# Performance work log

Measured on AMD Instinct MI355X. Metric: run time of the kernel, lower is better.

## Reference

```python
import jax, jax.numpy as jnp
import numpy as np

B, N, F = 32, 1024, 7
HID, HID_GLO, MLP_H, OUT = 256, 8, 64, 8
THRESHOLD = 0.3


def setup_inputs() -> dict:
    key = jax.random.key(0)
    ks = jax.random.split(key, 16)
    def lin(k, fan_out, fan_in):
        # xavier-uniform-like init
        lim = (6.0 / (fan_in + fan_out)) ** 0.5
        return jax.random.uniform(k, (fan_out, fan_in), jnp.float32, -lim, lim)
    return {
        "x": jax.random.normal(ks[0], (B, N, F), jnp.float32),
        "W1": lin(ks[1], HID, 2),   "b1": jnp.zeros((HID,), jnp.float32),
        "W2": lin(ks[2], HID, HID), "b2": jnp.zeros((HID,), jnp.float32),
        "Wfc": lin(ks[3], HID, HID), "bfc": jnp.zeros((HID,), jnp.float32),
        "Wg": lin(ks[4], HID_GLO, 2), "bg": jnp.zeros((HID_GLO,), jnp.float32),
        "Wm0": lin(ks[5], MLP_H, N * F), "bm0": jnp.zeros((MLP_H,), jnp.float32),
        "Wm1": lin(ks[6], MLP_H, MLP_H), "bm1": jnp.zeros((MLP_H,), jnp.float32),
        "Wp": lin(ks[7], OUT, MLP_H + HID + HID_GLO), "bp": jnp.zeros((OUT,), jnp.float32),
    }


def reference(x, W1, b1, W2, b2, Wfc, bfc, Wg, bg, Wm0, bm0, Wm1, bm1, Wp, bp):
    # --- GCN branch (torch code detaches node features & adjacency) ---
    pts = jax.lax.stop_gradient(x[:, :, 1:3])                     # [B,N,2]
    diff = pts[:, :, None, :] - pts[:, None, :, :]                # [B,N,N,2]
    dist = jnp.sqrt(jnp.sum(diff * diff, axis=-1))                # [B,N,N]
    adj = (dist < THRESHOLD).astype(x.dtype)                      # [B,N,N]
    dinv = 1.0 / jnp.sqrt(jnp.sum(adj, axis=-1))                  # [B,N] (>=1, self-loop)
    nadj = dinv[:, :, None] * adj * dinv[:, None, :]              # D^-1/2 A D^-1/2
    h = jax.nn.relu(jnp.einsum('bij,bjd->bid', nadj, pts) @ W1.T + b1)   # [B,N,256]
    g = jnp.einsum('bij,bjh->bih', nadj, h) @ W2.T + b2                  # [B,N,256]
    gcn_en = jnp.mean(g, axis=1) @ Wfc.T + bfc                    # [B,256]

    # --- global branch (torch code uses .item() -> constants) ---
    v = jax.lax.stop_gradient(x[:, :, 1:5])                       # [B,N,4]
    avg_speed = jnp.mean(jnp.linalg.norm(v[:, :, 2:4], axis=-1), axis=1)  # [B]
    density = 1.0 / jnp.max(dist, axis=(1, 2))                    # [B] (v3 == pts)
    glo_in = jnp.stack([avg_speed, density], axis=-1)             # [B,2]
    glo_en = jax.nn.relu(glo_in @ Wg.T + bg)                      # [B,8]

    # --- MLP branch on flattened x ---
    xf = x.reshape(x.shape[0], -1)                                # [B, N*F]
    xf = jax.nn.relu(xf @ Wm0.T + bm0)
    xf = jax.nn.relu(xf @ Wm1.T + bm1)                            # [B,64]

    out = jnp.concatenate([xf, gcn_en, glo_en], axis=1) @ Wp.T + bp  # [B,8]
    return out
```

## Files before the change

### kernel.cpp

```cpp
#include <hip/hip_runtime.h>

#define BB 32
#define NN 1024
#define FF 7
#define HID 256
#define MLPH 64
#define OUTN 8
#define CATN (MLPH + HID + 8)

__device__ __forceinline__ float wave_sum(float v) {
#pragma unroll
    for (int m = 32; m >= 1; m >>= 1) v += __shfl_xor(v, m, 64);
    return v;
}
__device__ __forceinline__ float wave_max(float v) {
#pragma unroll
    for (int m = 32; m >= 1; m >>= 1) v = fmaxf(v, __shfl_xor(v, m, 64));
    return v;
}

union S1 {
    struct { float xb[NN * FF]; float l0[NN], l1[NN], s2[NN], s3[NN]; float wred[16]; } a;
    struct { float xb[NN * FF]; float wred[16]; } p;
    struct { float l0[HID], l1[HID], r2[HID]; float wred[16]; } c;
    struct { float wb[NN * FF]; } m;
};

__global__ __launch_bounds__(1024, 4) void k1(const float* __restrict__ x,
                                              const float* __restrict__ Wm0,
                                              const float* __restrict__ W2,
                                              const float* __restrict__ b2,
                                              const float* __restrict__ Wfc,
                                              const float* __restrict__ bfc,
                                              const float* __restrict__ Wp,
                                              float* __restrict__ pts0,
                                              float* __restrict__ pts1,
                                              float* __restrict__ spd,
                                              float* __restrict__ mlp_p,
                                              float* __restrict__ E,
                                              float* __restrict__ cE,
                                              float* __restrict__ deg,
                                              float* __restrict__ bmaxp,
                                              float* __restrict__ out) {
    __shared__ __align__(16) S1 sm;
    int blk = blockIdx.x, tid = threadIdx.x, lane = tid & 63, w = tid >> 6;
    if (blk < 256) {
        int b = blk >> 3, jg = blk & 7;
        const float4* xr = (const float4*)(x + b * (NN * FF));
        float4* s4 = (float4*)sm.a.xb;
        for (int i = tid; i < 1792; i += 1024) s4[i] = xr[i];
        __syncthreads();
        sm.a.l0[tid] = sm.a.xb[tid * FF + 1];
        sm.a.l1[tid] = sm.a.xb[tid * FF + 2];
        __syncthreads();
        int jA = jg * 128 + lane, jB = jA + 64;
        float pj0a = sm.a.l0[jA], pj1a = sm.a.l1[jA];
        float pj0b = sm.a.l0[jB], pj1b = sm.a.l1[jB];
        const float4* v0p = (const float4*)&sm.a.l0[w * 64];
        const float4* v1p = (const float4*)&sm.a.l1[w * 64];
        unsigned dA = 0u, dB = 0u;
        float mx = 0.f;
#pragma unroll 4
        for (int g = 0; g < 16; ++g) {
            float4 v0 = v0p[g], v1 = v1p[g];
            float dx, dy, d2a, d2b;
            dx = pj0a - v0.x; dy = pj1a - v1.x; d2a = fmaf(dy, dy, dx * dx);
            dx = pj0b - v0.x; dy = pj1b - v1.x; d2b = fmaf(dy, dy, dx * dx);
            dA += (d2a <= 0.09f); dB += (d2b <= 0.09f);
            mx = fmaxf(mx, fmaxf(d2a, d2b));
            dx = pj0a - v0.y; dy = pj1a - v1.y; d2a = fmaf(dy, dy, dx * dx);
            dx = pj0b - v0.y; dy = pj1b - v1.y; d2b = fmaf(dy, dy, dx * dx);
            dA += (d2a <= 0.09f); dB += (d2b <= 0.09f);
            mx = fmaxf(mx, fmaxf(d2a, d2b));
            dx = pj0a - v0.z; dy = pj1a - v1.z; d2a = fmaf(dy, dy, dx * dx);
            dx = pj0b - v0.z; dy = pj1b - v1.z; d2b = fmaf(dy, dy, dx * dx);
            dA += (d2a <= 0.09f); dB += (d2b <= 0.09f);
            mx = fmaxf(mx, fmaxf(d2a, d2b));
            dx = pj0a - v0.w; dy = pj1a - v1.w; d2a = fmaf(dy, dy, dx * dx);
            dx = pj0b - v0.w; dy = pj1b - v1.w; d2b = fmaf(dy, dy, dx * dx);
            dA += (d2a <= 0.09f); dB += (d2b <= 0.09f);
            mx = fmaxf(mx, fmaxf(d2a, d2b));
        }
        sm.a.s2[tid] = (float)dA;
        sm.a.s3[tid] = (float)dB;
        mx = wave_max(mx);
        if (lane == 0) sm.a.wred[w] = mx;
        __syncthreads();
        if (tid < 64) {
            float s = 0.f;
#pragma unroll
            for (int kk = 0; kk < 16; ++kk) s += sm.a.s2[kk * 64 + tid];
            deg[b * NN + jg * 128 + tid] = s;
        } else if (tid < 128) {
            int t = tid - 64;
            float s = 0.f;
#pragma unroll
            for (int kk = 0; kk < 16; ++kk) s += sm.a.s3[kk * 64 + t];
            deg[b * NN + jg * 128 + 64 + t] = s;
        }
        if (tid == 0) {
            float m = sm.a.wred[0];
#pragma unroll
            for (int i = 1; i < 16; ++i) m = fmaxf(m, sm.a.wred[i]);
            bmaxp[b * 8 + jg] = m;
        }
    } else if (blk < 288) {
        int b = blk - 256;
        const float4* xr = (const float4*)(x + b * (NN * FF));
        float4* s4 = (float4*)sm.p.xb;
        for (int i = tid; i < 1792; i += 1024) s4[i] = xr[i];
        if (tid < OUTN) out[b * OUTN + tid] = 0.f;
        __syncthreads();
        pts0[b * NN + tid] = sm.p.xb[tid * FF + 1];
        pts1[b * NN + tid] = sm.p.xb[tid * FF + 2];
        float vx = sm.p.xb[tid * FF + 3], vy = sm.p.xb[tid * FF + 4];
        float sp = sqrtf(fmaf(vx, vx, vy * vy));
        sp = wave_sum(sp);
        if (lane == 0) sm.p.wred[w] = sp;
        __syncthreads();
        if (tid == 0) {
            float s = 0.f;
#pragma unroll
            for (int i = 0; i < 16; ++i) s += sm.p.wred[i];
            spd[b] = s;
        }
    } else if (blk < 296) {
        int o = blk - 288;
        if (tid < HID) sm.c.l0[tid] = Wp[o * CATN + MLPH + tid];
        __syncthreads();
        if (tid < HID) {
            float a = 0.f;
#pragma unroll 8
            for (int m = 0; m < HID; ++m) a = fmaf(sm.c.l0[m], Wfc[m * HID + tid], a);
            sm.c.l1[tid] = a;
            sm.c.r2[tid] = sm.c.l0[tid] * bfc[tid];
        }
        __syncthreads();
        if (tid < HID) {
            float e = 0.f;
#pragma unroll 8
            for (int k = 0; k < HID; ++k) e = fmaf(sm.c.l1[k], W2[k * HID + tid], e);
            E[o * HID + tid] = e;
            float c = fmaf(sm.c.l1[tid], b2[tid], sm.c.r2[tid]);
            c = wave_sum(c);
            if (lane == 0) sm.c.wred[w] = c;
        }
        __syncthreads();
        if (tid == 0) cE[o] = sm.c.wred[0] + sm.c.wred[1] + sm.c.wred[2] + sm.c.wred[3];
    } else {
        int t = blk - 296, h = t >> 1, half = t & 1;
        const float4* wr = (const float4*)(Wm0 + h * (NN * FF));
        float4* s4 = (float4*)sm.m.wb;
        for (int i = tid; i < 1792; i += 1024) s4[i] = wr[i];
        __syncthreads();
        int b = half * 16 + w;
        const float4* xr = (const float4*)(x + b * (NN * FF));
        float4 a4 = {0.f, 0.f, 0.f, 0.f};
#pragma unroll 7
        for (int it = 0; it < 28; ++it) {
            float4 xv = xr[it * 64 + lane];
            float4 wv = s4[it * 64 + lane];
            a4.x = fmaf(wv.x, xv.x, a4.x);
            a4.y = fmaf(wv.y, xv.y, a4.y);
            a4.z = fmaf(wv.z, xv.z, a4.z);
            a4.w = fmaf(wv.w, xv.w, a4.w);
        }
        float s = (a4.x + a4.y) + (a4.z + a4.w);
        s = wave_sum(s);
        if (lane == 0) mlp_p[b * MLPH + h] = s;
    }
}

struct S2 {
    float l0[NN], l1[NN], di[NN];
    float r0a[NN], r1a[NN], r2a[NN], r0b[NN], r1b[NN], r2b[NN];
    float q0[128], q1[128], qw[128];
};

__global__ __launch_bounds__(1024, 4) void k2(const float* __restrict__ pts0,
                                              const float* __restrict__ pts1,
                                              const float* __restrict__ deg,
                                              const float* __restrict__ W1,
                                              const float* __restrict__ b1,
                                              const float* __restrict__ Wg,
                                              const float* __restrict__ bg,
                                              const float* __restrict__ Wm1,
                                              const float* __restrict__ bm1,
                                              const float* __restrict__ Wp,
                                              const float* __restrict__ bp,
                                              const float* __restrict__ bm0,
                                              const float* __restrict__ mlp_p,
                                              const float* __restrict__ bmaxp,
                                              const float* __restrict__ spd,
                                              const float* __restrict__ E,
                                              const float* __restrict__ cE,
                                              float* __restrict__ out) {
    __shared__ __align__(16) S2 sm;
    int blk = blockIdx.x, tid = threadIdx.x, lane = tid & 63, w = tid >> 6;
    int b = blk >> 3, jg = blk & 7;
    float* hsl  = sm.l0;
    float* sx1  = sm.l1;
    float* sxf2 = sm.l1 + 64;
    float* sglo = sm.l1 + 128;
    sm.l0[tid] = pts0[b * NN + tid];
    sm.l1[tid] = pts1[b * NN + tid];
    sm.di[tid] = 1.0f / sqrtf(deg[b * NN + tid]);
    __syncthreads();
    int jA = jg * 128 + lane, jB = jA + 64;
    float pj0a = sm.l0[jA], pj1a = sm.l1[jA];
    float pj0b = sm.l0[jB], pj1b = sm.l1[jB];
    const float4* v0p = (const float4*)&sm.l0[w * 64];
    const float4* v1p = (const float4*)&sm.l1[w * 64];
    const float4* vdp = (const float4*)&sm.di[w * 64];
    float a0a = 0.f, a1a = 0.f, asa = 0.f;
    float a0b = 0.f, a1b = 0.f, asb = 0.f;
#pragma unroll 4
    for (int g = 0; g < 16; ++g) {
        float4 v0 = v0p[g], v1 = v1p[g], vd = vdp[g];
        float dx, dy, d2, t;
        dx = pj0a - v0.x; dy = pj1a - v1.x; d2 = fmaf(dy, dy, dx * dx);
        t = (d2 <= 0.09f) ? vd.x : 0.0f;
        a0a = fmaf(t, v0.x, a0a); a1a = fmaf(t, v1.x, a1a); asa += t;
        dx = pj0b - v0.x; dy = pj1b - v1.x; d2 = fmaf(dy, dy, dx * dx);
        t = (d2 <= 0.09f) ? vd.x : 0.0f;
        a0b = fmaf(t, v0.x, a0b); a1b = fmaf(t, v1.x, a1b); asb += t;
        dx = pj0a - v0.y; dy = pj1a - v1.y; d2 = fmaf(dy, dy, dx * dx);
        t = (d2 <= 0.09f) ? vd.y : 0.0f;
        a0a = fmaf(t, v0.y, a0a); a1a = fmaf(t, v1.y, a1a); asa += t;
        dx = pj0b - v0.y; dy = pj1b - v1.y; d2 = fmaf(dy, dy, dx * dx);
        t = (d2 <= 0.09f) ? vd.y : 0.0f;
        a0b = fmaf(t, v0.y, a0b); a1b = fmaf(t, v1.y, a1b); asb += t;
        dx = pj0a - v0.z; dy = pj1a - v1.z; d2 = fmaf(dy, dy, dx * dx);
        t = (d2 <= 0.09f) ? vd.z : 0.0f;
        a0a = fmaf(t, v0.z, a0a); a1a = fmaf(t, v1.z, a1a); asa += t;
        dx = pj0b - v0.z; dy = pj1b - v1.z; d2 = fmaf(dy, dy, dx * dx);
        t = (d2 <= 0.09f) ? vd.z : 0.0f;
        a0b = fmaf(t, v0.z, a0b); a1b = fmaf(t, v1.z, a1b); asb += t;
        dx = pj0a - v0.w; dy = pj1a - v1.w; d2 = fmaf(dy, dy, dx * dx);
        t = (d2 <= 0.09f) ? vd.w : 0.0f;
        a0a = fmaf(t, v0.w, a0a); a1a = fmaf(t, v1.w, a1a); asa += t;
        dx = pj0b - v0.w; dy = pj1b - v1.w; d2 = fmaf(dy, dy, dx * dx);
        t = (d2 <= 0.09f) ? vd.w : 0.0f;
        a0b = fmaf(t, v0.w, a0b); a1b = fmaf(t, v1.w, a1b); asb += t;
    }
    sm.r0a[tid] = a0a; sm.r1a[tid] = a1a; sm.r2a[tid] = asa;
    sm.r0b[tid] = a0b; sm.r1b[tid] = a1b; sm.r2b[tid] = asb;
    __syncthreads();
    if (tid < 128) {
        int t = tid & 63;
        const float* R0 = (tid < 64) ? sm.r0a : sm.r0b;
        const float* R1 = (tid < 64) ? sm.r1a : sm.r1b;
        const float* R2 = (tid < 64) ? sm.r2a : sm.r2b;
        int j = jg * 128 + tid;
        float s0 = 0.f, s1 = 0.f, ss = 0.f;
#pragma unroll
        for (int kk = 0; kk < 16; ++kk) {
            s0 += R0[kk * 64 + t];
            s1 += R1[kk * 64 + t];
            ss += R2[kk * 64 + t];
        }
        float dj = sm.di[j];
        sm.q0[tid] = dj * s0;
        sm.q1[tid] = dj * s1;
        sm.qw[tid] = dj * ss * (1.0f / NN);
    } else if (jg == 0 && tid < 192) {
        int t2 = tid - 128;
        sx1[t2] = fmaxf(mlp_p[b * MLPH + t2] + bm0[t2], 0.f);
    }
    __syncthreads();
    {
        int h = tid & 255, jq = tid >> 8;
        float w10 = W1[2 * h], w11 = W1[2 * h + 1], bb = b1[h];
        const float4* q0v = (const float4*)&sm.q0[jq * 32];
        const float4* q1v = (const float4*)&sm.q1[jq * 32];
        const float4* qwv = (const float4*)&sm.qw[jq * 32];
        float acc = 0.f;
#pragma unroll
        for (int g = 0; g < 8; ++g) {
            float4 qa = q0v[g], qb = q1v[g], qw4 = qwv[g];
            acc = fmaf(qw4.x, fmaxf(fmaf(qb.x, w11, fmaf(qa.x, w10, bb)), 0.f), acc);
            acc = fmaf(qw4.y, fmaxf(fmaf(qb.y, w11, fmaf(qa.y, w10, bb)), 0.f), acc);
            acc = fmaf(qw4.z, fmaxf(fmaf(qb.z, w11, fmaf(qa.z, w10, bb)), 0.f), acc);
            acc = fmaf(qw4.w, fmaxf(fmaf(qb.w, w11, fmaf(qa.w, w10, bb)), 0.f), acc);
        }
        sm.r0a[jq * 256 + h] = acc;
    }
    __syncthreads();
    if (tid < HID) {
        hsl[tid] = sm.r0a[tid] + sm.r0a[256 + tid] + sm.r0a[512 + tid] + sm.r0a[768 + tid];
    } else if (jg == 0 && tid < HID + MLPH) {
        int t2 = tid - HID;
        float a = bm1[t2];
        const float* wv = Wm1 + t2 * MLPH;
#pragma unroll
        for (int k = 0; k < MLPH; ++k) a = fmaf(wv[k], sx1[k], a);
        sxf2[t2] = fmaxf(a, 0.f);
    } else if (jg == 0 && tid < HID + MLPH + 8) {
        int t2 = tid - HID - MLPH;
        float mx = 0.f;
#pragma unroll
        for (int g = 0; g < 8; ++g) mx = fmaxf(mx, bmaxp[b * 8 + g]);
        float avg  = spd[b] * (1.0f / NN);
        float dens = 1.0f / sqrtf(mx);
        sglo[t2] = fmaxf(fmaf(Wg[t2 * 2], avg, fmaf(Wg[t2 * 2 + 1], dens, bg[t2])), 0.f);
    }
    __syncthreads();
    if (tid < 512) {
        int o = tid >> 6, ln = tid & 63;
        const float* Eo = E + o * HID;
        float a = Eo[ln] * hsl[ln];
        a = fmaf(Eo[ln + 64],  hsl[ln + 64],  a);
        a = fmaf(Eo[ln + 128], hsl[ln + 128], a);
        a = fmaf(Eo[ln + 192], hsl[ln + 192], a);
        if (jg == 0) a = fmaf(Wp[o * CATN + ln], sxf2[ln], a);
        a = wave_sum(a);
        if (ln == 0) {
            if (jg == 0) {
                const float* wg = Wp + o * CATN + MLPH + HID;
#pragma unroll
                for (int g = 0; g < 8; ++g) a = fmaf(wg[g], sglo[g], a);
                a += cE[o] + bp[o];
            }
            atomicAdd(&out[b * OUTN + o], a);
        }
    }
}

extern "C" void kernel_launch(void* const* d_in, const int* in_sizes, int n_in,
                              void* d_out, int out_size, void* d_ws, size_t ws_size,
                              hipStream_t stream) {
    const float* x   = (const float*)d_in[0];
    const float* W1  = (const float*)d_in[1];
    const float* b1  = (const float*)d_in[2];
    const float* W2  = (const float*)d_in[3];
    const float* b2  = (const float*)d_in[4];
    const float* Wfc = (const float*)d_in[5];
    const float* bfc = (const float*)d_in[6];
    const float* Wg  = (const float*)d_in[7];
    const float* bg  = (const float*)d_in[8];
    const float* Wm0 = (const float*)d_in[9];
    const float* bm0 = (const float*)d_in[10];
    const float* Wm1 = (const float*)d_in[11];
    const float* bm1 = (const float*)d_in[12];
    const float* Wp  = (const float*)d_in[13];
    const float* bp  = (const float*)d_in[14];
    float* out = (float*)d_out;
    float* ws  = (float*)d_ws;

    float* pts0  = ws;
    float* pts1  = ws + 32768;
    float* deg   = ws + 65536;
    float* mlp_p = ws + 98304;
    float* bmaxp = ws + 100352;
    float* spd   = ws + 100608;
    float* E     = ws + 100640;
    float* cE    = ws + 102688;

    k1<<<424, 1024, 0, stream>>>(x, Wm0, W2, b2, Wfc, bfc, Wp,
                                 pts0, pts1, spd, mlp_p, E, cE, deg, bmaxp, out);
    k2<<<256, 1024, 0, stream>>>(pts0, pts1, deg, W1, b1, Wg, bg, Wm1, bm1,
                                 Wp, bp, bm0, mlp_p, bmaxp, spd, E, cE, out);
}
```

Before: 123.5 us.

## Merge heterogeneous k1 block roles into uniform 512-thread blocks and drop pts buffers

Replaces the 424-block heterogeneous first kernel with 256 uniform 512-thread blocks. Each block now computes its degree slice, one MLP layer-0 dot product per wave, and optionally the speed sum and E precompute. The second kernel reads point coordinates straight from x instead of from pts0/pts1 workspace buffers, and both kernels halve their thread count and double the per-thread loop length. This is meant to cut the block count, the extra global round trip and the shared-memory footprint, at the cost of uncoalesced strided reads of x and Wm0 being reread per batch without shared staging.

```diff
diff --git a/kernel.cpp b/kernel.cpp
--- a/kernel.cpp
+++ b/kernel.cpp
@@ -1,6 +1,5 @@
 #include <hip/hip_runtime.h>
 
-#define BB 32
 #define NN 1024
 #define FF 7
 #define HID 256
@@ -19,203 +18,190 @@
     return v;
 }
 
-union S1 {
-    struct { float xb[NN * FF]; float l0[NN], l1[NN], s2[NN], s3[NN]; float wred[16]; } a;
-    struct { float xb[NN * FF]; float wred[16]; } p;
-    struct { float l0[HID], l1[HID], r2[HID]; float wred[16]; } c;
-    struct { float wb[NN * FF]; } m;
-};
-
-__global__ __launch_bounds__(1024, 4) void k1(const float* __restrict__ x,
-                                              const float* __restrict__ Wm0,
-                                              const float* __restrict__ W2,
-                                              const float* __restrict__ b2,
-                                              const float* __restrict__ Wfc,
-                                              const float* __restrict__ bfc,
-                                              const float* __restrict__ Wp,
-                                              float* __restrict__ pts0,
-                                              float* __restrict__ pts1,
-                                              float* __restrict__ spd,
-                                              float* __restrict__ mlp_p,
-                                              float* __restrict__ E,
-                                              float* __restrict__ cE,
-                                              float* __restrict__ deg,
-                                              float* __restrict__ bmaxp,
-                                              float* __restrict__ out) {
-    __shared__ __align__(16) S1 sm;
+__global__ __launch_bounds__(512, 4) void g1(const float* __restrict__ x,
+                                             const float* __restrict__ Wm0,
+                                             const float* __restrict__ W2,
+                                             const float* __restrict__ b2,
+                                             const float* __restrict__ Wfc,
+                                             const float* __restrict__ bfc,
+                                             const float* __restrict__ Wp,
+                                             float* __restrict__ spd,
+                                             float* __restrict__ mlp_p,
+                                             float* __restrict__ E,
+                                             float* __restrict__ cE,
+                                             float* __restrict__ deg,
+                                             float* __restrict__ bmaxp,
+                                             float* __restrict__ out) {
+    __shared__ __align__(16) float l0[NN];
+    __shared__ __align__(16) float l1[NN];
+    __shared__ __align__(16) float s2[8 * 128];
+    __shared__ float wred[8];
+    __shared__ float eg0[HID];
+    __shared__ float eg1[HID];
     int blk = blockIdx.x, tid = threadIdx.x, lane = tid & 63, w = tid >> 6;
-    if (blk < 256) {
-        int b = blk >> 3, jg = blk & 7;
-        const float4* xr = (const float4*)(x + b * (NN * FF));
-        float4* s4 = (float4*)sm.a.xb;
-        for (int i = tid; i < 1792; i += 1024) s4[i] = xr[i];
-        __syncthreads();
-        sm.a.l0[tid] = sm.a.xb[tid * FF + 1];
-        sm.a.l1[tid] = sm.a.xb[tid * FF + 2];
-        __syncthreads();
-        int jA = jg * 128 + lane, jB = jA + 64;
-        float pj0a = sm.a.l0[jA], pj1a = sm.a.l1[jA];
-        float pj0b = sm.a.l0[jB], pj1b = sm.a.l1[jB];
-        const float4* v0p = (const float4*)&sm.a.l0[w * 64];
-        const float4* v1p = (const float4*)&sm.a.l1[w * 64];
-        unsigned dA = 0u, dB = 0u;
-        float mx = 0.f;
+    int b = blk >> 3, jg = blk & 7;
+    const float* xb = x + b * (NN * FF);
+    {
+        int j0 = tid, j1 = tid + 512;
+        l0[j0] = xb[j0 * FF + 1]; l1[j0] = xb[j0 * FF + 2];
+        l0[j1] = xb[j1 * FF + 1]; l1[j1] = xb[j1 * FF + 2];
+    }
+    __syncthreads();
+    int jA = jg * 128 + lane, jB = jA + 64;
+    float pj0a = l0[jA], pj1a = l1[jA];
+    float pj0b = l0[jB], pj1b = l1[jB];
+    const float4* v0p = (const float4*)&l0[w * 128];
+    const float4* v1p = (const float4*)&l1[w * 128];
+    unsigned dA = 0u, dB = 0u;
+    float mx = 0.f;
 #pragma unroll 4
-        for (int g = 0; g < 16; ++g) {
-            float4 v0 = v0p[g], v1 = v1p[g];
-            float dx, dy, d2a, d2b;
-            dx = pj0a - v0.x; dy = pj1a - v1.x; d2a = fmaf(dy, dy, dx * dx);
-            dx = pj0b - v0.x; dy = pj1b - v1.x; d2b = fmaf(dy, dy, dx * dx);
-            dA += (d2a <= 0.09f); dB += (d2b <= 0.09f);
-            mx = fmaxf(mx, fmaxf(d2a, d2b));
-            dx = pj0a - v0.y; dy = pj1a - v1.y; d2a = fmaf(dy, dy, dx * dx);
-            dx = pj0b - v0.y; dy = pj1b - v1.y; d2b = fmaf(dy, dy, dx * dx);
-            dA += (d2a <= 0.09f); dB += (d2b <= 0.09f);
-            mx = fmaxf(mx, fmaxf(d2a, d2b));
-            dx = pj0a - v0.z; dy = pj1a - v1.z; d2a = fmaf(dy, dy, dx * dx);
-            dx = pj0b - v0.z; dy = pj1b - v1.z; d2b = fmaf(dy, dy, dx * dx);
-            dA += (d2a <= 0.09f); dB += (d2b <= 0.09f);
-            mx = fmaxf(mx, fmaxf(d2a, d2b));
-            dx = pj0a - v0.w; dy = pj1a - v1.w; d2a = fmaf(dy, dy, dx * dx);
-            dx = pj0b - v0.w; dy = pj1b - v1.w; d2b = fmaf(dy, dy, dx * dx);
-            dA += (d2a <= 0.09f); dB += (d2b <= 0.09f);
-            mx = fmaxf(mx, fmaxf(d2a, d2b));
-        }
-        sm.a.s2[tid] = (float)dA;
-        sm.a.s3[tid] = (float)dB;
-        mx = wave_max(mx);
-        if (lane == 0) sm.a.wred[w] = mx;
-        __syncthreads();
-        if (tid < 64) {
-            float s = 0.f;
-#pragma unroll
-            for (int kk = 0; kk < 16; ++kk) s += sm.a.s2[kk * 64 + tid];
-            deg[b * NN + jg * 128 + tid] = s;
-        } else if (tid < 128) {
-            int t = tid - 64;
-            float s = 0.f;
-#pragma unroll
-            for (int kk = 0; kk < 16; ++kk) s += sm.a.s3[kk * 64 + t];
-            deg[b * NN + jg * 128 + 64 + t] = s;
-        }
-        if (tid == 0) {
-            float m = sm.a.wred[0];
-#pragma unroll
-            for (int i = 1; i < 16; ++i) m = fmaxf(m, sm.a.wred[i]);
-            bmaxp[b * 8 + jg] = m;
-        }
-    } else if (blk < 288) {
-        int b = blk - 256;
-        const float4* xr = (const float4*)(x + b * (NN * FF));
-        float4* s4 = (float4*)sm.p.xb;
-        for (int i = tid; i < 1792; i += 1024) s4[i] = xr[i];
+    for (int g = 0; g < 32; ++g) {
+        float4 v0 = v0p[g], v1 = v1p[g];
+        float dx, dy, d2a, d2b;
+        dx = pj0a - v0.x; dy = pj1a - v1.x; d2a = fmaf(dy, dy, dx * dx);
+        dx = pj0b - v0.x; dy = pj1b - v1.x; d2b = fmaf(dy, dy, dx * dx);
+        dA += (d2a <= 0.09f); dB += (d2b <= 0.09f);
+        mx = fmaxf(mx, fmaxf(d2a, d2b));
+        dx = pj0a - v0.y; dy = pj1a - v1.y; d2a = fmaf(dy, dy, dx * dx);
+        dx = pj0b - v0.y; dy = pj1b - v1.y; d2b = fmaf(dy, dy, dx * dx);
+        dA += (d2a <= 0.09f); dB += (d2b <= 0.09f);
+        mx = fmaxf(mx, fmaxf(d2a, d2b));
+        dx = pj0a - v0.z; dy = pj1a - v1.z; d2a = fmaf(dy, dy, dx * dx);
+        dx = pj0b - v0.z; dy = pj1b - v1.z; d2b = fmaf(dy, dy, dx * dx);
+        dA += (d2a <= 0.09f); dB += (d2b <= 0.09f);
+        mx = fmaxf(mx, fmaxf(d2a, d2b));
+        dx = pj0a - v0.w; dy = pj1a - v1.w; d2a = fmaf(dy, dy, dx * dx);
+        dx = pj0b - v0.w; dy = pj1b - v1.w; d2b = fmaf(dy, dy, dx * dx);
+        dA += (d2a <= 0.09f); dB += (d2b <= 0.09f);
+        mx = fmaxf(mx, fmaxf(d2a, d2b));
+    }
+    s2[w * 128 + lane] = (float)dA;
+    s2[w * 128 + 64 + lane] = (float)dB;
+    mx = wave_max(mx);
+    if (lane == 0) wred[w] = mx;
+    __syncthreads();
+    if (tid < 128) {
+        float s = 0.f;
+#pragma unroll
+        for (int kk = 0; kk < 8; ++kk) s += s2[kk * 128 + tid];
+        deg[b * NN + jg * 128 + tid] = s;
+    }
+    if (tid == 0) {
+        float m = wred[0];
+#pragma unroll
+        for (int i = 1; i < 8; ++i) m = fmaxf(m, wred[i]);
+        bmaxp[b * 8 + jg] = m;
+    }
+    {
+        int h = jg * 8 + w;
+        const float4* wr = (const float4*)(Wm0 + h * (NN * FF));
+        const float4* xr = (const float4*)xb;
+        float4 a4 = {0.f, 0.f, 0.f, 0.f};
+#pragma unroll 7
+        for (int it = 0; it < 28; ++it) {
+            float4 wv = wr[it * 64 + lane];
+            float4 xv = xr[it * 64 + lane];
+            a4.x = fmaf(wv.x, xv.x, a4.x);
+            a4.y = fmaf(wv.y, xv.y, a4.y);
+            a4.z = fmaf(wv.z, xv.z, a4.z);
+            a4.w = fmaf(wv.w, xv.w, a4.w);
+        }
+        float s = (a4.x + a4.y) + (a4.z + a4.w);
+        s = wave_sum(s);
+        if (lane == 0) mlp_p[b * MLPH + h] = s;
+    }
+    __syncthreads();
+    if (jg == 0) {
+        int j0 = tid, j1 = tid + 512;
+        float vx = xb[j0 * FF + 3], vy = xb[j0 * FF + 4];
+        float sp = sqrtf(fmaf(vx, vx, vy * vy));
+        vx = xb[j1 * FF + 3]; vy = xb[j1 * FF + 4];
+        sp += sqrtf(fmaf(vx, vx, vy * vy));
+        sp = wave_sum(sp);
+        if (lane == 0) wred[w] = sp;
         if (tid < OUTN) out[b * OUTN + tid] = 0.f;
-        __syncthreads();
-        pts0[b * NN + tid] = sm.p.xb[tid * FF + 1];
-        pts1[b * NN + tid] = sm.p.xb[tid * FF + 2];
-        float vx = sm.p.xb[tid * FF + 3], vy = sm.p.xb[tid * FF + 4];
-        float sp = sqrtf(fmaf(vx, vx, vy * vy));
-        sp = wave_sum(sp);
-        if (lane == 0) sm.p.wred[w] = sp;
-        __syncthreads();
-        if (tid == 0) {
-            float s = 0.f;
-#pragma unroll
-            for (int i = 0; i < 16; ++i) s += sm.p.wred[i];
-            spd[b] = s;
-        }
-    } else if (blk < 296) {
-        int o = blk - 288;
-        if (tid < HID) sm.c.l0[tid] = Wp[o * CATN + MLPH + tid];
+    }
+    __syncthreads();
+    if (jg == 0 && tid == 0) {
+        float s = 0.f;
+#pragma unroll
+        for (int i = 0; i < 8; ++i) s += wred[i];
+        spd[b] = s;
+    }
+    if (b < 8 && jg == 7) {
+        int o = b;
+        if (tid < HID) eg0[tid] = Wp[o * CATN + MLPH + tid];
         __syncthreads();
         if (tid < HID) {
             float a = 0.f;
 #pragma unroll 8
-            for (int m = 0; m < HID; ++m) a = fmaf(sm.c.l0[m], Wfc[m * HID + tid], a);
-            sm.c.l1[tid] = a;
-            sm.c.r2[tid] = sm.c.l0[tid] * bfc[tid];
+            for (int m = 0; m < HID; ++m) a = fmaf(eg0[m], Wfc[m * HID + tid], a);
+            eg1[tid] = a;
         }
         __syncthreads();
         if (tid < HID) {
             float e = 0.f;
 #pragma unroll 8
-            for (int k = 0; k < HID; ++k) e = fmaf(sm.c.l1[k], W2[k * HID + tid], e);
+            for (int k = 0; k < HID; ++k) e = fmaf(eg1[k], W2[k * HID + tid], e);
             E[o * HID + tid] = e;
-            float c = fmaf(sm.c.l1[tid], b2[tid], sm.c.r2[tid]);
+            float c = fmaf(eg1[tid], b2[tid], eg0[tid] * bfc[tid]);
             c = wave_sum(c);
-            if (lane == 0) sm.c.wred[w] = c;
+            if (lane == 0) wred[w] = c;
         }
         __syncthreads();
-        if (tid == 0) cE[o] = sm.c.wred[0] + sm.c.wred[1] + sm.c.wred[2] + sm.c.wred[3];
-    } else {
-        int t = blk - 296, h = t >> 1, half = t & 1;
-        const float4* wr = (const float4*)(Wm0 + h * (NN * FF));
-        float4* s4 = (float4*)sm.m.wb;
-        for (int i = tid; i < 1792; i += 1024) s4[i] = wr[i];
-        __syncthreads();
-        int b = half * 16 + w;
-        const float4* xr = (const float4*)(x + b * (NN * FF));
-        float4 a4 = {0.f, 0.f, 0.f, 0.f};
-#pragma unroll 7
-        for (int it = 0; it < 28; ++it) {
-            float4 xv = xr[it * 64 + lane];
-            float4 wv = s4[it * 64 + lane];
-            a4.x = fmaf(wv.x, xv.x, a4.x);
-            a4.y = fmaf(wv.y, xv.y, a4.y);
-            a4.z = fmaf(wv.z, xv.z, a4.z);
-            a4.w = fmaf(wv.w, xv.w, a4.w);
-        }
-        float s = (a4.x + a4.y) + (a4.z + a4.w);
-        s = wave_sum(s);
-        if (lane == 0) mlp_p[b * MLPH + h] = s;
-    }
-}
-
-struct S2 {
-    float l0[NN], l1[NN], di[NN];
-    float r0a[NN], r1a[NN], r2a[NN], r0b[NN], r1b[NN], r2b[NN];
-    float q0[128], q1[128], qw[128];
-};
-
-__global__ __launch_bounds__(1024, 4) void k2(const float* __restrict__ pts0,
-                                              const float* __restrict__ pts1,
-                                              const float* __restrict__ deg,
-                                              const float* __restrict__ W1,
-                                              const float* __restrict__ b1,
-                                              const float* __restrict__ Wg,
-                                              const float* __restrict__ bg,
-                                              const float* __restrict__ Wm1,
-                                              const float* __restrict__ bm1,
-                                              const float* __restrict__ Wp,
-                                              const float* __restrict__ bp,
-                                              const float* __restrict__ bm0,
-                                              const float* __restrict__ mlp_p,
-                                              const float* __restrict__ bmaxp,
-                                              const float* __restrict__ spd,
-                                              const float* __restrict__ E,
-                                              const float* __restrict__ cE,
-                                              float* __restrict__ out) {
-    __shared__ __align__(16) S2 sm;
+        if (tid == 0) cE[o] = wred[0] + wred[1] + wred[2] + wred[3];
+    }
+}
+
+__global__ __launch_bounds__(512, 4) void g2(const float* __restrict__ x,
+                                             const float* __restrict__ deg,
+                                             const float* __restrict__ W1,
+                                             const float* __restrict__ b1,
+                                             const float* __restrict__ Wg,
+                                             const float* __restrict__ bg,
+                                             const float* __restrict__ Wm1,
+                                             const float* __restrict__ bm1,
+                                             const float* __restrict__ Wp,
+                                             const float* __restrict__ bp,
+                                             const float* __restrict__ bm0,
+                                             const float* __restrict__ mlp_p,
+                                             const float* __restrict__ bmaxp,
+                                             const float* __restrict__ spd,
+                                             const float* __restrict__ E,
+                                             const float* __restrict__ cE,
+                                             float* __restrict__ out) {
+    __shared__ __align__(16) float l0[NN];
+    __shared__ __align__(16) float l1[NN];
+    __shared__ __align__(16) float di[NN];
+    __shared__ __align__(16) float r0[8 * 128];
+    __shared__ __align__(16) float r1[8 * 128];
+    __shared__ __align__(16) float r2[8 * 128];
+    __shared__ __align__(16) float q0s[128];
+    __shared__ __align__(16) float q1s[128];
+    __shared__ __align__(16) float qws[128];
+    __shared__ __align__(16) float hp[512];
+    __shared__ float sx1[MLPH], sxf2[MLPH], sglo[8];
     int blk = blockIdx.x, tid = threadIdx.x, lane = tid & 63, w = tid >> 6;
     int b = blk >> 3, jg = blk & 7;
-    float* hsl  = sm.l0;
-    float* sx1  = sm.l1;
-    float* sxf2 = sm.l1 + 64;
-    float* sglo = sm.l1 + 128;
-    sm.l0[tid] = pts0[b * NN + tid];
-    sm.l1[tid] = pts1[b * NN + tid];
-    sm.di[tid] = 1.0f / sqrtf(deg[b * NN + tid]);
+    const float* xb = x + b * (NN * FF);
+    {
+        int j0 = tid, j1 = tid + 512;
+        l0[j0] = xb[j0 * FF + 1]; l1[j0] = xb[j0 * FF + 2];
+        l0[j1] = xb[j1 * FF + 1]; l1[j1] = xb[j1 * FF + 2];
+        di[j0] = 1.0f / sqrtf(deg[b * NN + j0]);
+        di[j1] = 1.0f / sqrtf(deg[b * NN + j1]);
+    }
     __syncthreads();
     int jA = jg * 128 + lane, jB = jA + 64;
-    float pj0a = sm.l0[jA], pj1a = sm.l1[jA];
-    float pj0b = sm.l0[jB], pj1b = sm.l1[jB];
-    const float4* v0p = (const float4*)&sm.l0[w * 64];
-    const float4* v1p = (const float4*)&sm.l1[w * 64];
-    const float4* vdp = (const float4*)&sm.di[w * 64];
+    float pj0a = l0[jA], pj1a = l1[jA];
+    float pj0b = l0[jB], pj1b = l1[jB];
+    const float4* v0p = (const float4*)&l0[w * 128];
+    const float4* v1p = (const float4*)&l1[w * 128];
+    const float4* vdp = (const float4*)&di[w * 128];
     float a0a = 0.f, a1a = 0.f, asa = 0.f;
     float a0b = 0.f, a1b = 0.f, asb = 0.f;
 #pragma unroll 4
-    for (int g = 0; g < 16; ++g) {
+    for (int g = 0; g < 32; ++g) {
         float4 v0 = v0p[g], v1 = v1p[g], vd = vdp[g];
         float dx, dy, d2, t;
         dx = pj0a - v0.x; dy = pj1a - v1.x; d2 = fmaf(dy, dy, dx * dx);
@@ -243,26 +229,22 @@
         t = (d2 <= 0.09f) ? vd.w : 0.0f;
         a0b = fmaf(t, v0.w, a0b); a1b = fmaf(t, v1.w, a1b); asb += t;
     }
-    sm.r0a[tid] = a0a; sm.r1a[tid] = a1a; sm.r2a[tid] = asa;
-    sm.r0b[tid] = a0b; sm.r1b[tid] = a1b; sm.r2b[tid] = asb;
+    r0[w * 128 + lane] = a0a; r0[w * 128 + 64 + lane] = a0b;
+    r1[w * 128 + lane] = a1a; r1[w * 128 + 64 + lane] = a1b;
+    r2[w * 128 + lane] = asa; r2[w * 128 + 64 + lane] = asb;
     __syncthreads();
     if (tid < 128) {
-        int t = tid & 63;
-        const float* R0 = (tid < 64) ? sm.r0a : sm.r0b;
-        const float* R1 = (tid < 64) ? sm.r1a : sm.r1b;
-        const float* R2 = (tid < 64) ? sm.r2a : sm.r2b;
-        int j = jg * 128 + tid;
         float s0 = 0.f, s1 = 0.f, ss = 0.f;
 #pragma unroll
-        for (int kk = 0; kk < 16; ++kk) {
-            s0 += R0[kk * 64 + t];
-            s1 += R1[kk * 64 + t];
-            ss += R2[kk * 64 + t];
-        }
-        float dj = sm.di[j];
-        sm.q0[tid] = dj * s0;
-        sm.q1[tid] = dj * s1;
-        sm.qw[tid] = dj * ss * (1.0f / NN);
+        for (int kk = 0; kk < 8; ++kk) {
+            s0 += r0[kk * 128 + tid];
+            s1 += r1[kk * 128 + tid];
+            ss += r2[kk * 128 + tid];
+        }
+        float dj = di[jg * 128 + tid];
+        q0s[tid] = dj * s0;
+        q1s[tid] = dj * s1;
+        qws[tid] = dj * ss * (1.0f / NN);
     } else if (jg == 0 && tid < 192) {
         int t2 = tid - 128;
         sx1[t2] = fmaxf(mlp_p[b * MLPH + t2] + bm0[t2], 0.f);
@@ -271,23 +253,23 @@
     {
         int h = tid & 255, jq = tid >> 8;
         float w10 = W1[2 * h], w11 = W1[2 * h + 1], bb = b1[h];
-        const float4* q0v = (const float4*)&sm.q0[jq * 32];
-        const float4* q1v = (const float4*)&sm.q1[jq * 32];
-        const float4* qwv = (const float4*)&sm.qw[jq * 32];
+        const float4* q0v = (const float4*)&q0s[jq * 64];
+        const float4* q1v = (const float4*)&q1s[jq * 64];
+        const float4* qwv = (const float4*)&qws[jq * 64];
         float acc = 0.f;
 #pragma unroll
-        for (int g = 0; g < 8; ++g) {
+        for (int g = 0; g < 16; ++g) {
             float4 qa = q0v[g], qb = q1v[g], qw4 = qwv[g];
             acc = fmaf(qw4.x, fmaxf(fmaf(qb.x, w11, fmaf(qa.x, w10, bb)), 0.f), acc);
             acc = fmaf(qw4.y, fmaxf(fmaf(qb.y, w11, fmaf(qa.y, w10, bb)), 0.f), acc);
             acc = fmaf(qw4.z, fmaxf(fmaf(qb.z, w11, fmaf(qa.z, w10, bb)), 0.f), acc);
             acc = fmaf(qw4.w, fmaxf(fmaf(qb.w, w11, fmaf(qa.w, w10, bb)), 0.f), acc);
         }
-        sm.r0a[jq * 256 + h] = acc;
+        hp[jq * 256 + h] = acc;
     }
     __syncthreads();
     if (tid < HID) {
-        hsl[tid] = sm.r0a[tid] + sm.r0a[256 + tid] + sm.r0a[512 + tid] + sm.r0a[768 + tid];
+        r0[tid] = hp[tid] + hp[256 + tid];
     } else if (jg == 0 && tid < HID + MLPH) {
         int t2 = tid - HID;
         float a = bm1[t2];
@@ -297,21 +279,21 @@
         sxf2[t2] = fmaxf(a, 0.f);
     } else if (jg == 0 && tid < HID + MLPH + 8) {
         int t2 = tid - HID - MLPH;
-        float mx = 0.f;
-#pragma unroll
-        for (int g = 0; g < 8; ++g) mx = fmaxf(mx, bmaxp[b * 8 + g]);
+        float mxv = 0.f;
+#pragma unroll
+        for (int g = 0; g < 8; ++g) mxv = fmaxf(mxv, bmaxp[b * 8 + g]);
         float avg  = spd[b] * (1.0f / NN);
-        float dens = 1.0f / sqrtf(mx);
+        float dens = 1.0f / sqrtf(mxv);
         sglo[t2] = fmaxf(fmaf(Wg[t2 * 2], avg, fmaf(Wg[t2 * 2 + 1], dens, bg[t2])), 0.f);
     }
     __syncthreads();
-    if (tid < 512) {
-        int o = tid >> 6, ln = tid & 63;
+    {
+        int o = w, ln = lane;
         const float* Eo = E + o * HID;
-        float a = Eo[ln] * hsl[ln];
-        a = fmaf(Eo[ln + 64],  hsl[ln + 64],  a);
-        a = fmaf(Eo[ln + 128], hsl[ln + 128], a);
-        a = fmaf(Eo[ln + 192], hsl[ln + 192], a);
+        float a = Eo[ln] * r0[ln];
+        a = fmaf(Eo[ln + 64],  r0[ln + 64],  a);
+        a = fmaf(Eo[ln + 128], r0[ln + 128], a);
+        a = fmaf(Eo[ln + 192], r0[ln + 192], a);
         if (jg == 0) a = fmaf(Wp[o * CATN + ln], sxf2[ln], a);
         a = wave_sum(a);
         if (ln == 0) {
@@ -347,17 +329,15 @@
     float* out = (float*)d_out;
     float* ws  = (float*)d_ws;
 
-    float* pts0  = ws;
-    float* pts1  = ws + 32768;
-    float* deg   = ws + 65536;
-    float* mlp_p = ws + 98304;
-    float* bmaxp = ws + 100352;
-    float* spd   = ws + 100608;
-    float* E     = ws + 100640;
-    float* cE    = ws + 102688;
-
-    k1<<<424, 1024, 0, stream>>>(x, Wm0, W2, b2, Wfc, bfc, Wp,
-                                 pts0, pts1, spd, mlp_p, E, cE, deg, bmaxp, out);
-    k2<<<256, 1024, 0, stream>>>(pts0, pts1, deg, W1, b1, Wg, bg, Wm1, bm1,
-                                 Wp, bp, bm0, mlp_p, bmaxp, spd, E, cE, out);
-}
+    float* deg   = ws;
+    float* mlp_p = ws + 32768;
+    float* bmaxp = ws + 34816;
+    float* spd   = ws + 35072;
+    float* E     = ws + 35104;
+    float* cE    = ws + 37152;
+
+    g1<<<256, 512, 0, stream>>>(x, Wm0, W2, b2, Wfc, bfc, Wp,
+                                spd, mlp_p, E, cE, deg, bmaxp, out);
+    g2<<<256, 512, 0, stream>>>(x, deg, W1, b1, Wg, bg, Wm1, bm1,
+                                Wp, bp, bm0, mlp_p, bmaxp, spd, E, cE, out);
+}
```

After: 124.8 us. Within noise of the previous version (+1.0%).
